# Kernel optimization log

Hardware: AMD Instinct MI355X
Metric: run time of the kernel (lower is better)

## Reference

```python
import jax, jax.numpy as jnp
import numpy as np

N_NODES = 200000
N_EDGES = 6400000
NUM_GRAPHS = 20000
D_NODE, D_EDGE, D_MSG = 5, 4, 10


def setup_inputs() -> dict:
    key = jax.random.key(0)
    ks = jax.random.split(key, 16)
    inp = {
        "edge_index": jax.random.randint(ks[0], (2, N_EDGES), 0, N_NODES, dtype=jnp.int64)
                      if jax.config.jax_enable_x64 else
                      jax.random.randint(ks[0], (2, N_EDGES), 0, N_NODES, dtype=jnp.int32),
        "node_attr": jax.random.normal(ks[1], (N_NODES, D_NODE), dtype=jnp.float32),
        "edge_attr": jax.random.normal(ks[2], (N_EDGES, D_EDGE), dtype=jnp.float32),
        "batch": jnp.sort(jax.random.randint(ks[3], (N_NODES,), 0, NUM_GRAPHS, dtype=jnp.int32)),
        "num_graphs": NUM_GRAPHS,
        # MPL_1: Linear(2*D_NODE + D_EDGE -> 10)
        "w_mpl": jax.random.normal(ks[4], (2 * D_NODE + D_EDGE, D_MSG), dtype=jnp.float32) * 0.3,
        "b_mpl": jnp.zeros((D_MSG,), dtype=jnp.float32),
        "w1": jax.random.normal(ks[5], (10, 10), dtype=jnp.float32) * 0.3,
        "b1": jnp.zeros((10,), dtype=jnp.float32),
        "w2": jax.random.normal(ks[6], (10, 5), dtype=jnp.float32) * 0.3,
        "b2": jnp.zeros((5,), dtype=jnp.float32),
        "w3": jax.random.normal(ks[7], (5, 5), dtype=jnp.float32) * 0.3,
        "b3": jnp.zeros((5,), dtype=jnp.float32),
        "w4": jax.random.normal(ks[8], (5, 1), dtype=jnp.float32) * 0.3,
        "b4": jnp.zeros((1,), dtype=jnp.float32),
    }
    return inp


def reference(edge_index, node_attr, edge_attr, batch, num_graphs,
              w_mpl, b_mpl, w1, b1, w2, b2, w3, b3, w4, b4):
    src, dst = edge_index[0], edge_index[1]
    n_nodes = node_attr.shape[0]
    # MPL_1: gather endpoints, concat with edge features, MLP, scatter-sum to dst
    edge_in = jnp.concatenate(
        [node_attr[src], node_attr[dst], edge_attr], axis=-1)  # [E, 14]
    msg = jax.nn.relu(edge_in @ w_mpl + b_mpl)                 # [E, 10]
    x = jax.ops.segment_sum(msg, dst, num_segments=n_nodes)    # [N, 10]
    # node MLP head
    x = jax.nn.relu(x @ w1 + b1)
    x = jax.nn.relu(x @ w2 + b2)
    # segment_coo(reduce='sum') over sorted batch index -> per-graph pooling
    x = jax.ops.segment_sum(x, batch, num_segments=num_graphs,
                            indices_are_sorted=True)           # [G, 5]
    x = jax.nn.relu(x @ w3 + b3)
    return x @ w4 + b4                                         # [G, 1]
```

## Files before the change

### kernel.cpp

```cpp
#include <hip/hip_runtime.h>
#include <hip/hip_fp16.h>

#define DN 5
#define DE 4
#define DM 10
#define NB 2048
#define BKT_SH 8
#define BKT_NODES 256
#define MAXBKT 1024

#define PERM(b) (((b) & 7) * (NB / 8) + ((b) >> 3))

typedef float        f4  __attribute__((ext_vector_type(4)));
typedef unsigned int u4v __attribute__((ext_vector_type(4)));

static __device__ __forceinline__ float2 h2f(unsigned u) {
    __half2 h = *reinterpret_cast<__half2*>(&u);
    return make_float2(__low2float(h), __high2float(h));
}
static __device__ __forceinline__ unsigned f2h(float a, float b) {
    __half2 h = __floats2half2_rn(a, b);
    return *reinterpret_cast<unsigned*>(&h);
}

__global__ __launch_bounds__(256) void hist_pack_kernel(
    const int* __restrict__ ei, const float* __restrict__ node_attr,
    u4v* __restrict__ naph, unsigned* __restrict__ cnt,
    int E, int chunk, int nbk, int N)
{
    __shared__ unsigned hist[MAXBKT];
    int t = threadIdx.x, b = blockIdx.x;

    int n = b * 256 + t;
    if (n < N) {
        const float* r = node_attr + (size_t)n * DN;
        u4v v;
        v.x = f2h(r[0], r[1]);
        v.y = f2h(r[2], r[3]);
        v.z = f2h(r[4], 0.f);
        v.w = 0u;
        naph[n] = v;
    }

    for (int j = t; j < nbk; j += 256) hist[j] = 0;
    __syncthreads();

    int e0 = b * chunk, e1 = min(E, e0 + chunk);
    for (int i = e0 + t; i < e1; i += 256) {
        int d = __builtin_nontemporal_load(ei + (size_t)E + i);
        atomicAdd(&hist[d >> BKT_SH], 1u);
    }
    __syncthreads();
    for (int j = t; j < nbk; j += 256)
        cnt[(size_t)j * NB + PERM(b)] = hist[j];
}

__global__ __launch_bounds__(256) void scan_rows_kernel(
    unsigned* __restrict__ cnt, unsigned* __restrict__ rowtotal)
{
    __shared__ unsigned lds[256];
    int j = blockIdx.x, t = threadIdx.x;
    unsigned* row = cnt + (size_t)j * NB;

    unsigned v[8], s = 0;
#pragma unroll
    for (int u = 0; u < 8; ++u) { v[u] = row[t * 8 + u]; s += v[u]; }
    lds[t] = s; __syncthreads();
#pragma unroll
    for (int o = 1; o < 256; o <<= 1) {
        unsigned add = (t >= o) ? lds[t - o] : 0u;
        __syncthreads();
        lds[t] += add;
        __syncthreads();
    }
    unsigned excl = lds[t] - s;
#pragma unroll
    for (int u = 0; u < 8; ++u) { row[t * 8 + u] = excl; excl += v[u]; }
    if (t == 255) rowtotal[j] = lds[255];
}

__global__ __launch_bounds__(1024) void scan_base_kernel(
    const unsigned* __restrict__ rowtotal, unsigned* __restrict__ gbase,
    int nbk, int E)
{
    __shared__ unsigned lds[1024];
    int t = threadIdx.x;
    unsigned v = (t < nbk) ? rowtotal[t] : 0u;
    lds[t] = v; __syncthreads();
#pragma unroll
    for (int o = 1; o < 1024; o <<= 1) {
        unsigned add = (t >= o) ? lds[t - o] : 0u;
        __syncthreads();
        lds[t] += add;
        __syncthreads();
    }
    unsigned excl = lds[t] - v;
    if (t < nbk)       gbase[t] = excl;
    else if (t == nbk) gbase[t] = (unsigned)E;
}

__global__ __launch_bounds__(256) void scatter_kernel(
    const int* __restrict__ ei, const float* __restrict__ edge_attr,
    const unsigned* __restrict__ cnt, const unsigned* __restrict__ gbase,
    u4v* __restrict__ rec, int E, int chunk, int nbk)
{
    __shared__ unsigned woff[MAXBKT];
    int t = threadIdx.x, b = blockIdx.x;
    for (int j = t; j < nbk; j += 256)
        woff[j] = gbase[j] + cnt[(size_t)j * NB + PERM(b)];
    __syncthreads();

    int e0 = b * chunk, e1 = min(E, e0 + chunk);
    for (int i0 = e0 + t; i0 < e1; i0 += 4 * 256) {
        int s[4], d[4]; f4 ea[4]; bool act[4];
#pragma unroll
        for (int u = 0; u < 4; ++u) {
            int i = i0 + u * 256;
            act[u] = (i < e1);
            if (act[u]) {
                s[u]  = __builtin_nontemporal_load(ei + i);
                d[u]  = __builtin_nontemporal_load(ei + (size_t)E + i);
                ea[u] = __builtin_nontemporal_load(
                            reinterpret_cast<const f4*>(edge_attr) + i);
            }
        }
#pragma unroll
        for (int u = 0; u < 4; ++u) {
            if (!act[u]) continue;
            unsigned p = atomicAdd(&woff[d[u] >> BKT_SH], 1u);
            u4v r;
            r.x = (unsigned)s[u] | ((unsigned)(d[u] & 255) << 18);
            r.y = f2h(ea[u].x, ea[u].y);
            r.z = f2h(ea[u].z, ea[u].w);
            r.w = 0u;
            rec[p] = r;
        }
    }
}

__global__ __launch_bounds__(256) void gather_kernel(
    const u4v* __restrict__ rec, const unsigned* __restrict__ gbase,
    const u4v* __restrict__ naph,
    const float* __restrict__ w_mpl, const float* __restrict__ b_mpl,
    float* __restrict__ xpart, size_t xstride,
    int E, int N, int nbk, int nsplit)
{
    __shared__ float acc[BKT_NODES * DM];
    __shared__ float pdl[BKT_NODES * 12];
    __shared__ float sws[50];
    __shared__ float swe[40];

    int t = threadIdx.x;
    int j  = blockIdx.x / nsplit;
    int sp = blockIdx.x - j * nsplit;
    int nb0 = j * BKT_NODES;

    if (t < 50)       sws[t] = w_mpl[t];
    else if (t < 90)  swe[t - 50] = w_mpl[100 + (t - 50)];

    for (int i = t; i < BKT_NODES * DM; i += 256) acc[i] = 0.f;

    {
        int n = nb0 + t;
        float a0 = 0.f, a1 = 0.f, a2 = 0.f, a3 = 0.f, a4 = 0.f;
        if (n < N) {
            u4v v = naph[n];
            float2 p01 = h2f(v.x), p23 = h2f(v.y), p4 = h2f(v.z);
            a0 = p01.x; a1 = p01.y; a2 = p23.x; a3 = p23.y; a4 = p4.x;
        }
#pragma unroll
        for (int q = 0; q < DM; ++q) {
            float v = b_mpl[q];
            v = fmaf(a0, w_mpl[50 + q], v);
            v = fmaf(a1, w_mpl[60 + q], v);
            v = fmaf(a2, w_mpl[70 + q], v);
            v = fmaf(a3, w_mpl[80 + q], v);
            v = fmaf(a4, w_mpl[90 + q], v);
            pdl[t * 12 + q] = v;
        }
    }
    __syncthreads();

    unsigned start = gbase[j];
    unsigned end   = gbase[j + 1];
    unsigned blen  = end - start;
    unsigned csz   = (blen + nsplit - 1) / nsplit;
    unsigned ss    = start + (unsigned)sp * csz;
    unsigned se    = min(end, ss + csz);

    for (unsigned i0 = ss + t; i0 < se; i0 += 4u * 256u) {
        u4v r[4]; bool act[4];
#pragma unroll
        for (int u = 0; u < 4; ++u) {
            unsigned i = i0 + (unsigned)u * 256u;
            act[u] = (i < se);
            if (act[u]) r[u] = __builtin_nontemporal_load(rec + i);
        }
        u4v nap[4];
#pragma unroll
        for (int u = 0; u < 4; ++u)
            if (act[u]) nap[u] = naph[r[u].x & 0x3FFFFu];
#pragma unroll
        for (int u = 0; u < 4; ++u) {
            if (!act[u]) continue;
            int dl = (int)((r[u].x >> 18) & 255u);
            float2 s01 = h2f(nap[u].x);
            float2 s23 = h2f(nap[u].y);
            float2 s4_ = h2f(nap[u].z);
            float2 e01 = h2f(r[u].y);
            float2 e23 = h2f(r[u].z);
            float a0 = s01.x, a1 = s01.y, a2 = s23.x, a3 = s23.y, a4 = s4_.x;
            float e0 = e01.x, e1 = e01.y, e2 = e23.x, e3 = e23.y;

            const float* pr = &pdl[dl * 12];
            float4 p0 = *reinterpret_cast<const float4*>(pr);
            float4 p1 = *reinterpret_cast<const float4*>(pr + 4);
            float2 p2 = *reinterpret_cast<const float2*>(pr + 8);
            float m[DM] = {p0.x, p0.y, p0.z, p0.w, p1.x, p1.y, p1.z, p1.w, p2.x, p2.y};
#pragma unroll
            for (int q = 0; q < DM; ++q) {
                float v = m[q];
                v = fmaf(a0, sws[q],      v);
                v = fmaf(a1, sws[10 + q], v);
                v = fmaf(a2, sws[20 + q], v);
                v = fmaf(a3, sws[30 + q], v);
                v = fmaf(a4, sws[40 + q], v);
                v = fmaf(e0, swe[q],      v);
                v = fmaf(e1, swe[10 + q], v);
                v = fmaf(e2, swe[20 + q], v);
                v = fmaf(e3, swe[30 + q], v);
                if (v > 0.f) atomicAdd(&acc[dl * DM + q], v);
            }
        }
    }
    __syncthreads();

    float* dst = xpart + (size_t)sp * xstride + (size_t)nb0 * DM;
    for (int i = t; i < BKT_NODES * DM; i += 256)
        __builtin_nontemporal_store(acc[i], dst + i);
}

__global__ __launch_bounds__(256) void combine_kernel(
    const float* __restrict__ xpart, size_t xstride,
    const int* __restrict__ batch,
    const float* __restrict__ w1, const float* __restrict__ b1,
    const float* __restrict__ w2, const float* __restrict__ b2,
    float* __restrict__ gacc, int N, int nsplit)
{
    __shared__ float s1[100], sb1[10], s2[50], sb2[5];
    int t = threadIdx.x;
    if (t < 100)      s1[t] = w1[t];
    else if (t < 110) sb1[t - 100] = b1[t - 100];
    else if (t < 160) s2[t - 110] = w2[t - 110];
    else if (t < 165) sb2[t - 160] = b2[t - 160];
    __syncthreads();

    int n = blockIdx.x * blockDim.x + t;
    bool valid = (n < N);
    int g = 0x7fffffff;
    float h2v[5] = {0.f, 0.f, 0.f, 0.f, 0.f};

    if (valid) {
        float x[DM];
#pragma unroll
        for (int q = 0; q < DM; ++q) x[q] = 0.f;
        for (int sp = 0; sp < nsplit; ++sp) {
            const float2* row = reinterpret_cast<const float2*>(
                xpart + (size_t)sp * xstride + (size_t)n * DM);
#pragma unroll
            for (int h = 0; h < 5; ++h) {
                float2 v = row[h];
                x[2 * h] += v.x; x[2 * h + 1] += v.y;
            }
        }

        float h1[10];
#pragma unroll
        for (int q = 0; q < 10; ++q) h1[q] = sb1[q];
#pragma unroll
        for (int k = 0; k < 10; ++k)
#pragma unroll
            for (int q = 0; q < 10; ++q) h1[q] = fmaf(x[k], s1[k * 10 + q], h1[q]);
#pragma unroll
        for (int q = 0; q < 10; ++q) h1[q] = fmaxf(h1[q], 0.f);
#pragma unroll
        for (int q = 0; q < 5; ++q) h2v[q] = sb2[q];
#pragma unroll
        for (int k = 0; k < 10; ++k)
#pragma unroll
            for (int q = 0; q < 5; ++q) h2v[q] = fmaf(h1[k], s2[k * 5 + q], h2v[q]);
#pragma unroll
        for (int q = 0; q < 5; ++q) h2v[q] = fmaxf(h2v[q], 0.f);
        g = batch[n];
    }

    int lane = t & 63;
#pragma unroll
    for (int o = 1; o < 64; o <<= 1) {
        int go = __shfl_down(g, o);
        float v0 = __shfl_down(h2v[0], o);
        float v1 = __shfl_down(h2v[1], o);
        float v2 = __shfl_down(h2v[2], o);
        float v3 = __shfl_down(h2v[3], o);
        float v4 = __shfl_down(h2v[4], o);
        if (lane + o < 64 && go == g) {
            h2v[0] += v0; h2v[1] += v1; h2v[2] += v2; h2v[3] += v3; h2v[4] += v4;
        }
    }
    int gp = __shfl_up(g, 1);
    bool head = (lane == 0) || (gp != g);
    if (head && g != 0x7fffffff) {
#pragma unroll
        for (int q = 0; q < 5; ++q)
            if (h2v[q] != 0.f) unsafeAtomicAdd(&gacc[(size_t)g * 5 + q], h2v[q]);
    }
}

__global__ __launch_bounds__(256) void graph_head_kernel(
    const float* __restrict__ gacc,
    const float* __restrict__ w3, const float* __restrict__ b3,
    const float* __restrict__ w4, const float* __restrict__ b4,
    float* __restrict__ out, int G)
{
    __shared__ float s3[25], sb3[5], s4[5], sb4[1];
    int t = threadIdx.x;
    if (t < 25)       s3[t] = w3[t];
    else if (t < 30)  sb3[t - 25] = b3[t - 25];
    else if (t < 35)  s4[t - 30] = w4[t - 30];
    else if (t == 35) sb4[0] = b4[0];
    __syncthreads();

    int g = blockIdx.x * blockDim.x + t;
    if (g >= G) return;

    float x[5];
#pragma unroll
    for (int k = 0; k < 5; ++k) x[k] = gacc[(size_t)g * 5 + k];

    float o = sb4[0];
#pragma unroll
    for (int q = 0; q < 5; ++q) {
        float h = sb3[q];
#pragma unroll
        for (int k = 0; k < 5; ++k) h = fmaf(x[k], s3[k * 5 + q], h);
        h = fmaxf(h, 0.f);
        o = fmaf(h, s4[q], o);
    }
    out[g] = o;
}

extern "C" void kernel_launch(void* const* d_in, const int* in_sizes, int n_in,
                              void* d_out, int out_size, void* d_ws, size_t ws_size,
                              hipStream_t stream)
{
    const int*   ei        = (const int*)d_in[0];
    const float* node_attr = (const float*)d_in[1];
    const float* edge_attr = (const float*)d_in[2];
    const int*   batch     = (const int*)d_in[3];
    const float* w_mpl = (const float*)d_in[5];
    const float* b_mpl = (const float*)d_in[6];
    const float* w1    = (const float*)d_in[7];
    const float* b1    = (const float*)d_in[8];
    const float* w2    = (const float*)d_in[9];
    const float* b2    = (const float*)d_in[10];
    const float* w3    = (const float*)d_in[11];
    const float* b3    = (const float*)d_in[12];
    const float* w4    = (const float*)d_in[13];
    const float* b4    = (const float*)d_in[14];
    float* out = (float*)d_out;

    const int E = in_sizes[0] / 2;
    const int N = in_sizes[1] / DN;
    const int G = out_size;

    const int nbk   = (N + BKT_NODES - 1) / BKT_NODES;
    const int chunk = (E + NB - 1) / NB;

    char* p = (char*)d_ws;
    u4v*      rec      = (u4v*)p;      p += (size_t)E * 16;
    u4v*      naph     = (u4v*)p;      p += (size_t)N * 16;
    unsigned* rowtotal = (unsigned*)p; p += ((size_t)nbk * 4 + 15) & ~15ull;
    unsigned* gbase    = (unsigned*)p; p += ((size_t)(nbk + 1) * 4 + 15) & ~15ull;
    float*    gacc     = (float*)p;    p += (size_t)G * 5 * 4;
    unsigned* cnt      = (unsigned*)p;
    float*    xpart    = (float*)p;
    size_t cnt_bytes = (size_t)nbk * NB * 4;

    size_t used = (size_t)((char*)cnt - (char*)d_ws);
    size_t xstride = (size_t)nbk * BKT_NODES * DM;
    int nsplit = 8;
    while (nsplit > 1 &&
           used + ((cnt_bytes > (size_t)nsplit * xstride * 4) ? cnt_bytes
                                                              : (size_t)nsplit * xstride * 4) > ws_size)
        nsplit >>= 1;

    hipMemsetAsync(gacc, 0, (size_t)G * 5 * 4, stream);

    hist_pack_kernel<<<NB, 256, 0, stream>>>(ei, node_attr, naph, cnt, E, chunk, nbk, N);
    scan_rows_kernel<<<nbk, 256, 0, stream>>>(cnt, rowtotal);
    scan_base_kernel<<<1, 1024, 0, stream>>>(rowtotal, gbase, nbk, E);
    scatter_kernel<<<NB, 256, 0, stream>>>(ei, edge_attr, cnt, gbase, rec, E, chunk, nbk);
    gather_kernel<<<nbk * nsplit, 256, 0, stream>>>(rec, gbase, naph, w_mpl, b_mpl,
                                                    xpart, xstride, E, N, nbk, nsplit);
    combine_kernel<<<nbk, 256, 0, stream>>>(xpart, xstride, batch, w1, b1, w2, b2, gacc, N, nsplit);
    graph_head_kernel<<<(G + 255) / 256, 256, 0, stream>>>(gacc, w3, b3, w4, b4, out, G);
}
```

Baseline: 506.4 us.

## Drop per-bucket split partials; one 512-thread block per bucket accumulates directly

Each destination bucket is now processed by a single 512-thread block with 8-way unrolled edge loads, instead of nsplit blocks writing separate partial accumulators. The combine kernel reads one accumulator instead of summing nsplit partials. This removes the partial-buffer writes and reads. The trade-off is fewer, larger blocks and more LDS atomic contention per bucket, which could reduce latency hiding on the irregular gathers.

```diff
diff --git a/kernel.cpp b/kernel.cpp
--- a/kernel.cpp
+++ b/kernel.cpp
@@ -138,12 +138,11 @@
     }
 }
 
-__global__ __launch_bounds__(256) void gather_kernel(
+__global__ __launch_bounds__(512) void gather_kernel(
     const u4v* __restrict__ rec, const unsigned* __restrict__ gbase,
     const u4v* __restrict__ naph,
     const float* __restrict__ w_mpl, const float* __restrict__ b_mpl,
-    float* __restrict__ xpart, size_t xstride,
-    int E, int N, int nbk, int nsplit)
+    float* __restrict__ xacc, int E, int N, int nbk)
 {
     __shared__ float acc[BKT_NODES * DM];
     __shared__ float pdl[BKT_NODES * 12];
@@ -151,16 +150,17 @@
     __shared__ float swe[40];
 
     int t = threadIdx.x;
-    int j  = blockIdx.x / nsplit;
-    int sp = blockIdx.x - j * nsplit;
+    int j = blockIdx.x;
     int nb0 = j * BKT_NODES;
 
-    if (t < 50)       sws[t] = w_mpl[t];
-    else if (t < 90)  swe[t - 50] = w_mpl[100 + (t - 50)];
-
-    for (int i = t; i < BKT_NODES * DM; i += 256) acc[i] = 0.f;
-
-    {
+    if (t >= 512 - 96) {
+        int w = t - (512 - 96);
+        if (w < 50)      sws[w] = w_mpl[w];
+        else if (w < 90) swe[w - 50] = w_mpl[100 + (w - 50)];
+    }
+    for (int i = t; i < BKT_NODES * DM; i += 512) acc[i] = 0.f;
+
+    if (t < BKT_NODES) {
         int n = nb0 + t;
         float a0 = 0.f, a1 = 0.f, a2 = 0.f, a3 = 0.f, a4 = 0.f;
         if (n < N) {
@@ -181,27 +181,23 @@
     }
     __syncthreads();
 
-    unsigned start = gbase[j];
-    unsigned end   = gbase[j + 1];
-    unsigned blen  = end - start;
-    unsigned csz   = (blen + nsplit - 1) / nsplit;
-    unsigned ss    = start + (unsigned)sp * csz;
-    unsigned se    = min(end, ss + csz);
-
-    for (unsigned i0 = ss + t; i0 < se; i0 += 4u * 256u) {
-        u4v r[4]; bool act[4];
-#pragma unroll
-        for (int u = 0; u < 4; ++u) {
-            unsigned i = i0 + (unsigned)u * 256u;
+    unsigned ss = gbase[j];
+    unsigned se = gbase[j + 1];
+
+    for (unsigned i0 = ss + t; i0 < se; i0 += 8u * 512u) {
+        u4v r[8]; bool act[8];
+#pragma unroll
+        for (int u = 0; u < 8; ++u) {
+            unsigned i = i0 + (unsigned)u * 512u;
             act[u] = (i < se);
             if (act[u]) r[u] = __builtin_nontemporal_load(rec + i);
         }
-        u4v nap[4];
-#pragma unroll
-        for (int u = 0; u < 4; ++u)
+        u4v nap[8];
+#pragma unroll
+        for (int u = 0; u < 8; ++u)
             if (act[u]) nap[u] = naph[r[u].x & 0x3FFFFu];
 #pragma unroll
-        for (int u = 0; u < 4; ++u) {
+        for (int u = 0; u < 8; ++u) {
             if (!act[u]) continue;
             int dl = (int)((r[u].x >> 18) & 255u);
             float2 s01 = h2f(nap[u].x);
@@ -235,17 +231,17 @@
     }
     __syncthreads();
 
-    float* dst = xpart + (size_t)sp * xstride + (size_t)nb0 * DM;
-    for (int i = t; i < BKT_NODES * DM; i += 256)
+    float* dst = xacc + (size_t)nb0 * DM;
+    for (int i = t; i < BKT_NODES * DM; i += 512)
         __builtin_nontemporal_store(acc[i], dst + i);
 }
 
 __global__ __launch_bounds__(256) void combine_kernel(
-    const float* __restrict__ xpart, size_t xstride,
+    const float* __restrict__ xacc,
     const int* __restrict__ batch,
     const float* __restrict__ w1, const float* __restrict__ b1,
     const float* __restrict__ w2, const float* __restrict__ b2,
-    float* __restrict__ gacc, int N, int nsplit)
+    float* __restrict__ gacc, int N)
 {
     __shared__ float s1[100], sb1[10], s2[50], sb2[5];
     int t = threadIdx.x;
@@ -262,16 +258,11 @@
 
     if (valid) {
         float x[DM];
-#pragma unroll
-        for (int q = 0; q < DM; ++q) x[q] = 0.f;
-        for (int sp = 0; sp < nsplit; ++sp) {
-            const float2* row = reinterpret_cast<const float2*>(
-                xpart + (size_t)sp * xstride + (size_t)n * DM);
-#pragma unroll
-            for (int h = 0; h < 5; ++h) {
-                float2 v = row[h];
-                x[2 * h] += v.x; x[2 * h + 1] += v.y;
-            }
+        const float2* row = reinterpret_cast<const float2*>(xacc + (size_t)n * DM);
+#pragma unroll
+        for (int h = 0; h < 5; ++h) {
+            float2 v = row[h];
+            x[2 * h] = v.x; x[2 * h + 1] = v.y;
         }
 
         float h1[10];
@@ -382,17 +373,8 @@
     unsigned* rowtotal = (unsigned*)p; p += ((size_t)nbk * 4 + 15) & ~15ull;
     unsigned* gbase    = (unsigned*)p; p += ((size_t)(nbk + 1) * 4 + 15) & ~15ull;
     float*    gacc     = (float*)p;    p += (size_t)G * 5 * 4;
-    unsigned* cnt      = (unsigned*)p;
-    float*    xpart    = (float*)p;
-    size_t cnt_bytes = (size_t)nbk * NB * 4;
-
-    size_t used = (size_t)((char*)cnt - (char*)d_ws);
-    size_t xstride = (size_t)nbk * BKT_NODES * DM;
-    int nsplit = 8;
-    while (nsplit > 1 &&
-           used + ((cnt_bytes > (size_t)nsplit * xstride * 4) ? cnt_bytes
-                                                              : (size_t)nsplit * xstride * 4) > ws_size)
-        nsplit >>= 1;
+    unsigned* cnt      = (unsigned*)p; p += (size_t)nbk * NB * 4;
+    float*    xacc     = (float*)p;    p += (size_t)nbk * BKT_NODES * DM * 4;
 
     hipMemsetAsync(gacc, 0, (size_t)G * 5 * 4, stream);
 
@@ -400,8 +382,7 @@
     scan_rows_kernel<<<nbk, 256, 0, stream>>>(cnt, rowtotal);
     scan_base_kernel<<<1, 1024, 0, stream>>>(rowtotal, gbase, nbk, E);
     scatter_kernel<<<NB, 256, 0, stream>>>(ei, edge_attr, cnt, gbase, rec, E, chunk, nbk);
-    gather_kernel<<<nbk * nsplit, 256, 0, stream>>>(rec, gbase, naph, w_mpl, b_mpl,
-                                                    xpart, xstride, E, N, nbk, nsplit);
-    combine_kernel<<<nbk, 256, 0, stream>>>(xpart, xstride, batch, w1, b1, w2, b2, gacc, N, nsplit);
+    gather_kernel<<<nbk, 512, 0, stream>>>(rec, gbase, naph, w_mpl, b_mpl, xacc, E, N, nbk);
+    combine_kernel<<<(N + 255) / 256, 256, 0, stream>>>(xacc, batch, w1, b1, w2, b2, gacc, N);
     graph_head_kernel<<<(G + 255) / 256, 256, 0, stream>>>(gacc, w3, b3, w4, b4, out, G);
 }
```

Result: slower. 562.2 us (+11.0%).
